# Performance work log

Measured on AMD Instinct MI355X. Metric: run time of the kernel, lower is better.

Reference implementation:

```python
import jax, jax.numpy as jnp
import numpy as np

N_NODES = 100000
N_EDGES = 1600000
H_FEATS = 128
OUT_CLASSES = 6


def setup_inputs() -> dict:
    key = jax.random.key(0)
    ks = jax.random.split(key, 9)
    h = jax.random.normal(ks[0], (N_NODES, H_FEATS), dtype=jnp.float32)
    src = jax.random.randint(ks[1], (N_EDGES,), 0, N_NODES)
    dst = jax.random.randint(ks[2], (N_EDGES,), 0, N_NODES)
    # torch nn.Linear convention: y = x @ W.T + b, W shape [out, in]
    W1 = jax.random.normal(ks[3], (64, 2 * H_FEATS), dtype=jnp.float32) * 0.05
    b1 = jax.random.normal(ks[4], (64,), dtype=jnp.float32) * 0.05
    W2 = jax.random.normal(ks[5], (32, 64), dtype=jnp.float32) * 0.05
    b2 = jax.random.normal(ks[6], (32,), dtype=jnp.float32) * 0.05
    W3 = jax.random.normal(ks[7], (OUT_CLASSES, 32), dtype=jnp.float32) * 0.05
    b3 = jax.random.normal(ks[8], (OUT_CLASSES,), dtype=jnp.float32) * 0.05
    return {"h": h, "src": src, "dst": dst, "W1": W1, "b1": b1,
            "W2": W2, "b2": b2, "W3": W3, "b3": b3}


def reference(h, src, dst, W1, b1, W2, b2, W3, b3):
    # Per-edge gather of src/dst node features, concat -> [E, 2*H]
    x = jnp.concatenate([h[src], h[dst]], axis=1)
    x = jax.nn.relu(x @ W1.T + b1)   # [E, 64]
    x = jax.nn.relu(x @ W2.T + b2)   # [E, 32]
    return x @ W3.T + b3             # [E, output_class]
```

## Files before the change

### kernel.cpp

```cpp
#include <hip/hip_runtime.h>
#include <hip/hip_bf16.h>
#include <stdint.h>


#define H 128

typedef short bf16x8 __attribute__((ext_vector_type(8)));
typedef float f32x4  __attribute__((ext_vector_type(4)));

__device__ __forceinline__ uint16_t f2bf(float f) {
    uint32_t u = __float_as_uint(f);
    return (uint16_t)((u + 0x7fffu + ((u >> 16) & 1u)) >> 16);
}
__device__ __forceinline__ uint32_t pk_bf16(float lo, float hi) {
    __hip_bfloat162 v = __float22bfloat162_rn(float2{lo, hi});
    return *reinterpret_cast<uint32_t*>(&v);
}
__device__ __forceinline__ uint32_t bfadd2_relu(uint32_t a, uint32_t b) {
    __hip_bfloat162 x = *reinterpret_cast<__hip_bfloat162*>(&a);
    __hip_bfloat162 y = *reinterpret_cast<__hip_bfloat162*>(&b);
    __hip_bfloat162 s = __hadd2(x, y);
    uint32_t zu = 0u;
    __hip_bfloat162 zero = *reinterpret_cast<__hip_bfloat162*>(&zu);
    __hip_bfloat162 r = __hmax2(s, zero);
    return *reinterpret_cast<uint32_t*>(&r);
}

__global__ void prep_weights(const float* __restrict__ W1,
                             const float* __restrict__ W2,
                             const float* __restrict__ W3,
                             uint16_t* __restrict__ Bfrag,
                             uint16_t* __restrict__ EFrag)
{
    int t = blockIdx.x * blockDim.x + threadIdx.x;
    int stride = gridDim.x * blockDim.x;
    for (int i = t; i < 4 * 8 * 64 * 8; i += stride) {
        int j    = i & 7;
        int lane = (i >> 3) & 63;
        int nt   = (i >> 9) & 7;
        int kt   = (i >> 12);
        int k = kt * 32 + (lane >> 4) * 8 + j;
        int n = nt * 16 + (lane & 15);
        float v = (n < 64) ? W1[n * 256 + k] : W1[(n - 64) * 256 + 128 + k];
        Bfrag[i] = f2bf(v);
    }
    for (int i = t; i < 5 * 64 * 8; i += stride) {
        int j    = i & 7;
        int lane = (i >> 3) & 63;
        int f    = i >> 9;
        uint16_t v;
        if (f < 4) {
            int kt = f >> 1, nt = f & 1;
            int k = kt * 32 + (lane >> 4) * 8 + j;
            int n = nt * 16 + (lane & 15);
            v = f2bf(W2[n * 64 + k]);
        } else {
            int k = (lane >> 4) * 8 + j;
            int n = lane & 15;
            v = (n < 6) ? f2bf(W3[n * 32 + k]) : (uint16_t)0;
        }
        EFrag[i] = v;
    }
}

__global__ void __launch_bounds__(256) node_gemm(
    const float* __restrict__ h,
    const uint16_t* __restrict__ Bfrag,
    const float* __restrict__ b1,
    uint16_t* __restrict__ pre, int N)
{
    const int wave = threadIdx.x >> 6;
    const int lane = threadIdx.x & 63;
    const int n0 = (blockIdx.x * 4 + wave) * 32;
    if (n0 >= N) return;

    const int m    = lane & 15;
    const int quad = lane >> 4;

    bf16x8 afr[2][4];
#pragma unroll
    for (int mt = 0; mt < 2; mt++) {
        int arow = n0 + mt * 16 + m; if (arow >= N) arow = N - 1;
        const float* hrow = h + (size_t)arow * H + quad * 8;
#pragma unroll
        for (int kt = 0; kt < 4; kt++) {
            float4 lo = *(const float4*)(hrow + kt * 32);
            float4 hi = *(const float4*)(hrow + kt * 32 + 4);
            union { bf16x8 v; uint32_t u[4]; } A;
            A.u[0] = pk_bf16(lo.x, lo.y); A.u[1] = pk_bf16(lo.z, lo.w);
            A.u[2] = pk_bf16(hi.x, hi.y); A.u[3] = pk_bf16(hi.z, hi.w);
            afr[mt][kt] = A.v;
        }
    }

#pragma unroll
    for (int nt = 0; nt < 8; nt++) {
        const int n = nt * 16 + m;
        f32x4 acc0 = {0.f, 0.f, 0.f, 0.f};
        f32x4 acc1 = {0.f, 0.f, 0.f, 0.f};
#pragma unroll
        for (int kt = 0; kt < 4; kt++) {
            bf16x8 bfr = *(const bf16x8*)(Bfrag + ((size_t)(kt * 8 + nt) * 64 + lane) * 8);
            acc0 = __builtin_amdgcn_mfma_f32_16x16x32_bf16(afr[0][kt], bfr, acc0, 0, 0, 0);
            acc1 = __builtin_amdgcn_mfma_f32_16x16x32_bf16(afr[1][kt], bfr, acc1, 0, 0, 0);
        }
        const float bv = (n < 64) ? b1[n] : 0.f;
#pragma unroll
        for (int r = 0; r < 4; r++) {
            const int node0 = n0 + quad * 4 + r;
            if (node0 < N) pre[(size_t)node0 * H + n] = f2bf(acc0[r] + bv);
            const int node1 = n0 + 16 + quad * 4 + r;
            if (node1 < N) pre[(size_t)node1 * H + n] = f2bf(acc1[r] + bv);
        }
    }
}

__global__ void __launch_bounds__(256, 2) edge_mlp(
    const uint16_t* __restrict__ pre,
    const int* __restrict__ src, const int* __restrict__ dst,
    const uint16_t* __restrict__ EFrag,
    const float* __restrict__ b2, const float* __restrict__ b3,
    float* __restrict__ out, long E)
{
    __shared__ uint16_t zbuf[4][64 * 40];

    const int wave = threadIdx.x >> 6;
    const int lane = threadIdx.x & 63;
    const int m15  = lane & 15;
    const int quad = lane >> 4;
    uint16_t* zw = &zbuf[wave][0];

    bf16x8 bL2[4], bL3;
#pragma unroll
    for (int f = 0; f < 4; f++) bL2[f] = *(const bf16x8*)(EFrag + (f * 64 + lane) * 8);
    bL3 = *(const bf16x8*)(EFrag + (4 * 64 + lane) * 8);
    const float vb2a = b2[m15];
    const float vb2b = b2[16 + m15];
    const float vb3  = (m15 < 6) ? b3[m15] : 0.f;

    const long e0 = (long)(blockIdx.x * 4 + wave) * 64;
    if (e0 >= E) return;

    const char* preb = (const char*)pre;
    uint32_t oa0, oa1, oa2, oa3, ob0, ob1, ob2, ob3;
    {
        long ea = e0 + m15;
        long eb = (ea + 16 < E) ? ea + 16 : E - 1;
        long ec = (ea + 32 < E) ? ea + 32 : E - 1;
        long ed = (ea + 48 < E) ? ea + 48 : E - 1;
        if (ea >= E) ea = E - 1;
        oa0 = (uint32_t)src[ea] * 256u + (uint32_t)quad * 16u;
        ob0 = (uint32_t)dst[ea] * 256u + 128u + (uint32_t)quad * 16u;
        oa1 = (uint32_t)src[eb] * 256u + (uint32_t)quad * 16u;
        ob1 = (uint32_t)dst[eb] * 256u + 128u + (uint32_t)quad * 16u;
        oa2 = (uint32_t)src[ec] * 256u + (uint32_t)quad * 16u;
        ob2 = (uint32_t)dst[ec] * 256u + 128u + (uint32_t)quad * 16u;
        oa3 = (uint32_t)src[ed] * 256u + (uint32_t)quad * 16u;
        ob3 = (uint32_t)dst[ed] * 256u + 128u + (uint32_t)quad * 16u;
    }
    uint4 a00 = *(const uint4*)(preb + oa0);
    uint4 a01 = *(const uint4*)(preb + oa0 + 64);
    uint4 b00 = *(const uint4*)(preb + ob0);
    uint4 b01 = *(const uint4*)(preb + ob0 + 64);
    uint4 a10 = *(const uint4*)(preb + oa1);
    uint4 a11 = *(const uint4*)(preb + oa1 + 64);
    uint4 b10 = *(const uint4*)(preb + ob1);
    uint4 b11 = *(const uint4*)(preb + ob1 + 64);
    uint4 a20 = *(const uint4*)(preb + oa2);
    uint4 a21 = *(const uint4*)(preb + oa2 + 64);
    uint4 b20 = *(const uint4*)(preb + ob2);
    uint4 b21 = *(const uint4*)(preb + ob2 + 64);
    uint4 a30 = *(const uint4*)(preb + oa3);
    uint4 a31 = *(const uint4*)(preb + oa3 + 64);
    uint4 b30 = *(const uint4*)(preb + ob3);
    uint4 b31 = *(const uint4*)(preb + ob3 + 64);

    __builtin_amdgcn_sched_barrier(0);

#define DO_SUBTILE(ST, UA0, UB0, UA1, UB1)                                        \
    {                                                                             \
        union { bf16x8 v; uint32_t u[4]; } A0, A1;                                \
        A0.u[0] = bfadd2_relu(UA0.x, UB0.x);                                      \
        A0.u[1] = bfadd2_relu(UA0.y, UB0.y);                                      \
        A0.u[2] = bfadd2_relu(UA0.z, UB0.z);                                      \
        A0.u[3] = bfadd2_relu(UA0.w, UB0.w);                                      \
        A1.u[0] = bfadd2_relu(UA1.x, UB1.x);                                      \
        A1.u[1] = bfadd2_relu(UA1.y, UB1.y);                                      \
        A1.u[2] = bfadd2_relu(UA1.z, UB1.z);                                      \
        A1.u[3] = bfadd2_relu(UA1.w, UB1.w);                                      \
        _Pragma("unroll")                                                         \
        for (int nt = 0; nt < 2; nt++) {                                          \
            f32x4 acc = {0.f, 0.f, 0.f, 0.f};                                     \
            acc = __builtin_amdgcn_mfma_f32_16x16x32_bf16(A0.v, bL2[nt], acc, 0, 0, 0); \
            acc = __builtin_amdgcn_mfma_f32_16x16x32_bf16(A1.v, bL2[2 + nt], acc, 0, 0, 0); \
            const float vb2 = nt ? vb2b : vb2a;                                   \
            _Pragma("unroll")                                                     \
            for (int r = 0; r < 4; r++) {                                         \
                float z = fmaxf(acc[r] + vb2, 0.f);                               \
                zw[((ST) * 16 + quad * 4 + r) * 40 + nt * 16 + m15] = f2bf(z);    \
            }                                                                     \
        }                                                                         \
    }

    DO_SUBTILE(0, a00, b00, a01, b01)
    DO_SUBTILE(1, a10, b10, a11, b11)
    DO_SUBTILE(2, a20, b20, a21, b21)
    DO_SUBTILE(3, a30, b30, a31, b31)
#undef DO_SUBTILE

#pragma unroll
    for (int st = 0; st < 4; st++) {
        bf16x8 a3 = *(const bf16x8*)(zw + (st * 16 + m15) * 40 + quad * 8);
        f32x4 o = {0.f, 0.f, 0.f, 0.f};
        o = __builtin_amdgcn_mfma_f32_16x16x32_bf16(a3, bL3, o, 0, 0, 0);
        if (m15 < 6) {
#pragma unroll
            for (int r = 0; r < 4; r++) {
                long e = e0 + st * 16 + quad * 4 + r;
                if (e < E) out[e * 6 + m15] = o[r] + vb3;
            }
        }
    }
}

extern "C" void kernel_launch(void* const* d_in, const int* in_sizes, int n_in,
                              void* d_out, int out_size, void* d_ws, size_t ws_size,
                              hipStream_t stream) {
    const float* h   = (const float*)d_in[0];
    const int*   src = (const int*)d_in[1];
    const int*   dst = (const int*)d_in[2];
    const float* W1  = (const float*)d_in[3];
    const float* b1  = (const float*)d_in[4];
    const float* W2  = (const float*)d_in[5];
    const float* b2  = (const float*)d_in[6];
    const float* W3  = (const float*)d_in[7];
    const float* b3  = (const float*)d_in[8];

    const int  N = in_sizes[0] / H;
    const long E = in_sizes[1];

    char* ws = (char*)d_ws;
    uint16_t* Bfrag = (uint16_t*)ws;
    uint16_t* EFrag = (uint16_t*)(ws + 64 * 1024);
    uint16_t* pre   = (uint16_t*)(ws + 128 * 1024);

    prep_weights<<<64, 256, 0, stream>>>(W1, W2, W3, Bfrag, EFrag);
    node_gemm<<<(N + 127) / 128, 256, 0, stream>>>(h, Bfrag, b1, pre, N);
    const int eblocks = (int)((E + 255) / 256);
    edge_mlp<<<eblocks, 256, 0, stream>>>(pre, src, dst, EFrag, b2, b3,
                                          (float*)d_out, E);
}
```

Baseline: 186.4 us.

## Pipeline edge gathers through double-buffered async LDS copies in persistent edge kernel

```diff
diff --git a/kernel.cpp b/kernel.cpp
--- a/kernel.cpp
+++ b/kernel.cpp
@@ -7,6 +7,12 @@
 
 typedef short bf16x8 __attribute__((ext_vector_type(8)));
 typedef float f32x4  __attribute__((ext_vector_type(4)));
+
+typedef const __attribute__((address_space(1))) void gas_void;
+typedef __attribute__((address_space(3))) void las_void;
+__device__ __forceinline__ void async_copy16(const void* g, void* l) {
+    __builtin_amdgcn_global_load_lds((gas_void*)g, (las_void*)l, 16, 0, 0);
+}
 
 __device__ __forceinline__ uint16_t f2bf(float f) {
     uint32_t u = __float_as_uint(f);
@@ -50,10 +56,11 @@
         int f    = i >> 9;
         uint16_t v;
         if (f < 4) {
-            int kt = f >> 1, nt = f & 1;
-            int k = kt * 32 + (lane >> 4) * 8 + j;
-            int n = nt * 16 + (lane & 15);
-            v = f2bf(W2[n * 64 + k]);
+            int nt = f >> 1, kt = f & 1;
+            int m  = lane & 15;
+            int row = (m >> 2) * 8 + (m & 3) + 4 * nt;
+            int col = kt * 32 + (lane >> 4) * 8 + j;
+            v = f2bf(W2[row * 64 + col]);
         } else {
             int k = (lane >> 4) * 8 + j;
             int n = lane & 15;
@@ -115,112 +122,140 @@
     }
 }
 
-__global__ void __launch_bounds__(256, 2) edge_mlp(
+__global__ void __launch_bounds__(128) edge_mlp(
     const uint16_t* __restrict__ pre,
     const int* __restrict__ src, const int* __restrict__ dst,
     const uint16_t* __restrict__ EFrag,
     const float* __restrict__ b2, const float* __restrict__ b3,
     float* __restrict__ out, long E)
 {
-    __shared__ uint16_t zbuf[4][64 * 40];
+    __shared__ char stage[2][2][8192];
 
     const int wave = threadIdx.x >> 6;
     const int lane = threadIdx.x & 63;
     const int m15  = lane & 15;
     const int quad = lane >> 4;
-    uint16_t* zw = &zbuf[wave][0];
-
-    bf16x8 bL2[4], bL3;
-#pragma unroll
-    for (int f = 0; f < 4; f++) bL2[f] = *(const bf16x8*)(EFrag + (f * 64 + lane) * 8);
+
+    char* bufs[2] = { &stage[wave][0][0], &stage[wave][1][0] };
+
+    bf16x8 w2a[4], bL3;
+#pragma unroll
+    for (int f = 0; f < 4; f++) w2a[f] = *(const bf16x8*)(EFrag + (f * 64 + lane) * 8);
     bL3 = *(const bf16x8*)(EFrag + (4 * 64 + lane) * 8);
-    const float vb2a = b2[m15];
-    const float vb2b = b2[16 + m15];
-    const float vb3  = (m15 < 6) ? b3[m15] : 0.f;
-
-    const long e0 = (long)(blockIdx.x * 4 + wave) * 64;
-    if (e0 >= E) return;
+    float vb2j[8];
+    {
+        float4 t0 = *(const float4*)(b2 + quad * 8);
+        float4 t1 = *(const float4*)(b2 + quad * 8 + 4);
+        vb2j[0] = t0.x; vb2j[1] = t0.y; vb2j[2] = t0.z; vb2j[3] = t0.w;
+        vb2j[4] = t1.x; vb2j[5] = t1.y; vb2j[6] = t1.z; vb2j[7] = t1.w;
+    }
+    const float vb3 = (m15 < 6) ? b3[m15] : 0.f;
+
+    const long ngroups = (E + 31) / 32;
+    const long wid = (long)blockIdx.x * 2 + wave;
+    const long nw  = (long)gridDim.x * 2;
+    if (wid >= ngroups) return;
 
     const char* preb = (const char*)pre;
-    uint32_t oa0, oa1, oa2, oa3, ob0, ob1, ob2, ob3;
+    const uint32_t q16 = (uint32_t)quad * 16u;
+
+#define LOADIDX(G, S0, S1, D0, D1)                                              \
+    {                                                                           \
+        long _e0 = (G) * 32;                                                    \
+        long _ea = _e0 + m15;      if (_ea >= E) _ea = E - 1;                   \
+        long _eb = _e0 + 16 + m15; if (_eb >= E) _eb = E - 1;                   \
+        S0 = (uint32_t)src[_ea] * 256u;                                         \
+        S1 = (uint32_t)src[_eb] * 256u;                                         \
+        D0 = (uint32_t)dst[_ea] * 256u + 128u;                                  \
+        D1 = (uint32_t)dst[_eb] * 256u + 128u;                                  \
+    }
+
+#define ISSUE(S0, S1, D0, D1, BUF)                                              \
+    {                                                                           \
+        async_copy16(preb + S0 + q16,       (BUF) + 0 * 1024);                  \
+        async_copy16(preb + S0 + 64 + q16,  (BUF) + 1 * 1024);                  \
+        async_copy16(preb + D0 + q16,       (BUF) + 2 * 1024);                  \
+        async_copy16(preb + D0 + 64 + q16,  (BUF) + 3 * 1024);                  \
+        async_copy16(preb + S1 + q16,       (BUF) + 4 * 1024);                  \
+        async_copy16(preb + S1 + 64 + q16,  (BUF) + 5 * 1024);                  \
+        async_copy16(preb + D1 + q16,       (BUF) + 6 * 1024);                  \
+        async_copy16(preb + D1 + 64 + q16,  (BUF) + 7 * 1024);                  \
+    }
+
+    uint32_t i1s0, i1s1, i1d0, i1d1;
     {
-        long ea = e0 + m15;
-        long eb = (ea + 16 < E) ? ea + 16 : E - 1;
-        long ec = (ea + 32 < E) ? ea + 32 : E - 1;
-        long ed = (ea + 48 < E) ? ea + 48 : E - 1;
-        if (ea >= E) ea = E - 1;
-        oa0 = (uint32_t)src[ea] * 256u + (uint32_t)quad * 16u;
-        ob0 = (uint32_t)dst[ea] * 256u + 128u + (uint32_t)quad * 16u;
-        oa1 = (uint32_t)src[eb] * 256u + (uint32_t)quad * 16u;
-        ob1 = (uint32_t)dst[eb] * 256u + 128u + (uint32_t)quad * 16u;
-        oa2 = (uint32_t)src[ec] * 256u + (uint32_t)quad * 16u;
-        ob2 = (uint32_t)dst[ec] * 256u + 128u + (uint32_t)quad * 16u;
-        oa3 = (uint32_t)src[ed] * 256u + (uint32_t)quad * 16u;
-        ob3 = (uint32_t)dst[ed] * 256u + 128u + (uint32_t)quad * 16u;
-    }
-    uint4 a00 = *(const uint4*)(preb + oa0);
-    uint4 a01 = *(const uint4*)(preb + oa0 + 64);
-    uint4 b00 = *(const uint4*)(preb + ob0);
-    uint4 b01 = *(const uint4*)(preb + ob0 + 64);
-    uint4 a10 = *(const uint4*)(preb + oa1);
-    uint4 a11 = *(const uint4*)(preb + oa1 + 64);
-    uint4 b10 = *(const uint4*)(preb + ob1);
-    uint4 b11 = *(const uint4*)(preb + ob1 + 64);
-    uint4 a20 = *(const uint4*)(preb + oa2);
-    uint4 a21 = *(const uint4*)(preb + oa2 + 64);
-    uint4 b20 = *(const uint4*)(preb + ob2);
-    uint4 b21 = *(const uint4*)(preb + ob2 + 64);
-    uint4 a30 = *(const uint4*)(preb + oa3);
-    uint4 a31 = *(const uint4*)(preb + oa3 + 64);
-    uint4 b30 = *(const uint4*)(preb + ob3);
-    uint4 b31 = *(const uint4*)(preb + ob3 + 64);
-
-    __builtin_amdgcn_sched_barrier(0);
-
-#define DO_SUBTILE(ST, UA0, UB0, UA1, UB1)                                        \
-    {                                                                             \
-        union { bf16x8 v; uint32_t u[4]; } A0, A1;                                \
-        A0.u[0] = bfadd2_relu(UA0.x, UB0.x);                                      \
-        A0.u[1] = bfadd2_relu(UA0.y, UB0.y);                                      \
-        A0.u[2] = bfadd2_relu(UA0.z, UB0.z);                                      \
-        A0.u[3] = bfadd2_relu(UA0.w, UB0.w);                                      \
-        A1.u[0] = bfadd2_relu(UA1.x, UB1.x);                                      \
-        A1.u[1] = bfadd2_relu(UA1.y, UB1.y);                                      \
-        A1.u[2] = bfadd2_relu(UA1.z, UB1.z);                                      \
-        A1.u[3] = bfadd2_relu(UA1.w, UB1.w);                                      \
-        _Pragma("unroll")                                                         \
-        for (int nt = 0; nt < 2; nt++) {                                          \
-            f32x4 acc = {0.f, 0.f, 0.f, 0.f};                                     \
-            acc = __builtin_amdgcn_mfma_f32_16x16x32_bf16(A0.v, bL2[nt], acc, 0, 0, 0); \
-            acc = __builtin_amdgcn_mfma_f32_16x16x32_bf16(A1.v, bL2[2 + nt], acc, 0, 0, 0); \
-            const float vb2 = nt ? vb2b : vb2a;                                   \
-            _Pragma("unroll")                                                     \
-            for (int r = 0; r < 4; r++) {                                         \
-                float z = fmaxf(acc[r] + vb2, 0.f);                               \
-                zw[((ST) * 16 + quad * 4 + r) * 40 + nt * 16 + m15] = f2bf(z);    \
-            }                                                                     \
-        }                                                                         \
-    }
-
-    DO_SUBTILE(0, a00, b00, a01, b01)
-    DO_SUBTILE(1, a10, b10, a11, b11)
-    DO_SUBTILE(2, a20, b20, a21, b21)
-    DO_SUBTILE(3, a30, b30, a31, b31)
-#undef DO_SUBTILE
-
-#pragma unroll
-    for (int st = 0; st < 4; st++) {
-        bf16x8 a3 = *(const bf16x8*)(zw + (st * 16 + m15) * 40 + quad * 8);
-        f32x4 o = {0.f, 0.f, 0.f, 0.f};
-        o = __builtin_amdgcn_mfma_f32_16x16x32_bf16(a3, bL3, o, 0, 0, 0);
-        if (m15 < 6) {
-#pragma unroll
-            for (int r = 0; r < 4; r++) {
-                long e = e0 + st * 16 + quad * 4 + r;
-                if (e < E) out[e * 6 + m15] = o[r] + vb3;
+        uint32_t s0, s1, d0, d1;
+        LOADIDX(wid, s0, s1, d0, d1)
+        ISSUE(s0, s1, d0, d1, bufs[0])
+        long g1 = wid + nw; if (g1 >= ngroups) g1 = ngroups - 1;
+        LOADIDX(g1, i1s0, i1s1, i1d0, i1d1)
+    }
+
+    int p = 0;
+    for (long g = wid; g < ngroups; g += nw) {
+        char* bufc = bufs[p];
+        char* bufn = bufs[p ^ 1];
+        const long gn = g + nw;
+
+        uint4 ra[2][2], rb[2][2];
+#pragma unroll
+        for (int st = 0; st < 2; st++) {
+#pragma unroll
+            for (int kt = 0; kt < 2; kt++) {
+                ra[st][kt] = *(const uint4*)(bufc + ((st * 2 + 0) * 2 + kt) * 1024 + lane * 16);
+                rb[st][kt] = *(const uint4*)(bufc + ((st * 2 + 1) * 2 + kt) * 1024 + lane * 16);
             }
         }
-    }
+
+        if (gn < ngroups) {
+            uint32_t s0 = i1s0, s1 = i1s1, d0 = i1d0, d1 = i1d1;
+            ISSUE(s0, s1, d0, d1, bufn)
+        }
+        {
+            long g2 = gn + nw; if (g2 >= ngroups) g2 = ngroups - 1;
+            LOADIDX(g2, i1s0, i1s1, i1d0, i1d1)
+        }
+        __builtin_amdgcn_sched_barrier(0);
+
+#pragma unroll
+        for (int st = 0; st < 2; st++) {
+            union { bf16x8 v; uint32_t u[4]; } Y0, Y1;
+            Y0.u[0] = bfadd2_relu(ra[st][0].x, rb[st][0].x);
+            Y0.u[1] = bfadd2_relu(ra[st][0].y, rb[st][0].y);
+            Y0.u[2] = bfadd2_relu(ra[st][0].z, rb[st][0].z);
+            Y0.u[3] = bfadd2_relu(ra[st][0].w, rb[st][0].w);
+            Y1.u[0] = bfadd2_relu(ra[st][1].x, rb[st][1].x);
+            Y1.u[1] = bfadd2_relu(ra[st][1].y, rb[st][1].y);
+            Y1.u[2] = bfadd2_relu(ra[st][1].z, rb[st][1].z);
+            Y1.u[3] = bfadd2_relu(ra[st][1].w, rb[st][1].w);
+
+            f32x4 z0 = {0.f, 0.f, 0.f, 0.f};
+            f32x4 z1 = {0.f, 0.f, 0.f, 0.f};
+            z0 = __builtin_amdgcn_mfma_f32_16x16x32_bf16(w2a[0], Y0.v, z0, 0, 0, 0);
+            z0 = __builtin_amdgcn_mfma_f32_16x16x32_bf16(w2a[1], Y1.v, z0, 0, 0, 0);
+            z1 = __builtin_amdgcn_mfma_f32_16x16x32_bf16(w2a[2], Y0.v, z1, 0, 0, 0);
+            z1 = __builtin_amdgcn_mfma_f32_16x16x32_bf16(w2a[3], Y1.v, z1, 0, 0, 0);
+
+            union { bf16x8 v; uint32_t u[4]; } A3;
+            A3.u[0] = pk_bf16(fmaxf(z0[0] + vb2j[0], 0.f), fmaxf(z0[1] + vb2j[1], 0.f));
+            A3.u[1] = pk_bf16(fmaxf(z0[2] + vb2j[2], 0.f), fmaxf(z0[3] + vb2j[3], 0.f));
+            A3.u[2] = pk_bf16(fmaxf(z1[0] + vb2j[4], 0.f), fmaxf(z1[1] + vb2j[5], 0.f));
+            A3.u[3] = pk_bf16(fmaxf(z1[2] + vb2j[6], 0.f), fmaxf(z1[3] + vb2j[7], 0.f));
+
+            f32x4 o = {0.f, 0.f, 0.f, 0.f};
+            o = __builtin_amdgcn_mfma_f32_16x16x32_bf16(A3.v, bL3, o, 0, 0, 0);
+            if (m15 < 6) {
+#pragma unroll
+                for (int r = 0; r < 4; r++) {
+                    long e = g * 32 + st * 16 + quad * 4 + r;
+                    if (e < E) out[(size_t)e * 6 + m15] = o[r] + vb3;
+                }
+            }
+        }
+        p ^= 1;
+    }
+#undef LOADIDX
+#undef ISSUE
 }
 
 extern "C" void kernel_launch(void* const* d_in, const int* in_sizes, int n_in,
@@ -246,7 +281,6 @@
 
     prep_weights<<<64, 256, 0, stream>>>(W1, W2, W3, Bfrag, EFrag);
     node_gemm<<<(N + 127) / 128, 256, 0, stream>>>(h, Bfrag, b1, pre, N);
-    const int eblocks = (int)((E + 255) / 256);
-    edge_mlp<<<eblocks, 256, 0, stream>>>(pre, src, dst, EFrag, b2, b3,
-                                          (float*)d_out, E);
-}
+    edge_mlp<<<2048, 128, 0, stream>>>(pre, src, dst, EFrag, b2, b3,
+                                       (float*)d_out, E);
+}
```

Measured after the change: 207.1 us. 1.11x slower.
